# Kernel optimization log

Measured on AMD Instinct MI355X. Metric: run time of the kernel, lower is better.

Reference implementation:

```python
import jax, jax.numpy as jnp
import numpy as np

B, N, D = 4, 4096, 3
Q = jnp.array([0.05, 0.95, 0.25, 0.75], dtype=jnp.float32)  # q_begin + q_end


def _nn_diff(S1, S2):
    # For each point in S1 find nearest point in S2 (squared L2), return S1 - closest_S2.
    # d2: [N, N] built via the ||a||^2 + ||b||^2 - 2ab expansion (avoids [N,N,D]).
    d2 = (jnp.sum(S1 * S1, axis=-1, keepdims=True)
          + jnp.sum(S2 * S2, axis=-1)[None, :]
          - 2.0 * (S1 @ S2.T))
    idx = jnp.argmin(d2, axis=1)          # [N] nearest index in S2
    return S1 - S2[idx]                   # [N, D] vector residuals (mean=False path)


def _masked_std(v, mask):
    # torch.std over the masked subset (unbiased, correction=1), mask is float {0,1}.
    n = jnp.sum(mask)
    mean = jnp.sum(v * mask) / n
    var = jnp.sum(mask * (v - mean) ** 2) / (n - 1.0)
    return jnp.sqrt(var)


def _mask_std_pair(d):
    # mask_by_Z: quantiles computed under no_grad (stop_gradient), then std of each subset.
    v = d.reshape(-1)
    q = jnp.quantile(jax.lax.stop_gradient(v), Q.astype(v.dtype))
    mask_begin = ((v < q[0]) | (v > q[1])).astype(v.dtype)
    mask_end = ((v > q[2]) & (v < q[3])).astype(v.dtype)
    return _masked_std(v, mask_begin), _masked_std(v, mask_end)


def _sigma_distance(S1, S2):
    d12 = _nn_diff(S1, S2)  # S1 -> S2 residuals
    d21 = _nn_diff(S2, S1)  # S2 -> S1 residuals
    b1, e1 = _mask_std_pair(d12)
    b2, e2 = _mask_std_pair(d21)
    return jnp.maximum(b1, b2), jnp.maximum(e1, e2)


def setup_inputs() -> dict:
    key = jax.random.key(0)
    kx, ky = jax.random.split(key)
    x = jax.random.normal(kx, (B, N, D), dtype=jnp.float32)
    y = jax.random.normal(ky, (B, N, D), dtype=jnp.float32)
    return {"x": x, "y": y}


def reference(x, y):
    begin, end = jax.vmap(_sigma_distance)(x, y)  # [B], [B]
    return begin.mean(), end.mean()
```

## Files before the change

### kernel.cpp

```cpp
#include <hip/hip_runtime.h>
#include <math.h>

constexpr int B_  = 4;
constexpr int N_  = 4096;
constexpr int NV  = N_ * 3;
constexpr int QPT = 8;
constexpr int TPB_TAIL = 1024;

__device__ inline unsigned f2k(float f) {
    unsigned b = __float_as_uint(f);
    return b ^ ((unsigned)((int)b >> 31) | 0x80000000u);
}
__device__ inline float k2f(unsigned k) {
    unsigned b = (k & 0x80000000u) ? (k ^ 0x80000000u) : ~k;
    return __uint_as_float(b);
}

template <int NCCH>
__global__ __launch_bounds__(256, 2) void nn_partial_kernel(const float* __restrict__ x,
                                                            const float* __restrict__ y,
                                                            float2* __restrict__ part) {
    constexpr int CCH = N_ / NCCH;
    __shared__ float4 s2[CCH];
    const int pair = blockIdx.z;
    const int b    = pair >> 1;
    const int dir  = pair & 1;
    const float* S1 = (dir == 0 ? x : y) + b * NV;
    const float* S2 = (dir == 0 ? y : x) + b * NV;
    const int cbase = blockIdx.x * CCH;

    for (int j = threadIdx.x; j < CCH; j += 256) {
        float bx = S2[(cbase + j) * 3 + 0];
        float by = S2[(cbase + j) * 3 + 1];
        float bz = S2[(cbase + j) * 3 + 2];
        s2[j] = make_float4(-2.f * bx, -2.f * by, -2.f * bz,
                            bx * bx + by * by + bz * bz);
    }
    __syncthreads();

    const int q0 = blockIdx.y * 2048 + threadIdx.x * QPT;
    float ax[QPT], ay[QPT], az[QPT];
    {
        const float4* p4 = (const float4*)(S1 + q0 * 3);
        float4 v[6];
        #pragma unroll
        for (int i = 0; i < 6; ++i) v[i] = p4[i];
        const float* f = (const float*)v;
        #pragma unroll
        for (int k = 0; k < QPT; ++k) {
            ax[k] = f[k * 3 + 0]; ay[k] = f[k * 3 + 1]; az[k] = f[k * 3 + 2];
        }
    }

    float bd[QPT]; int idx[QPT];
    #pragma unroll
    for (int k = 0; k < QPT; ++k) { bd[k] = INFINITY; idx[k] = 0; }

    for (int j = 0; j < CCH; ++j) {
        float4 c = s2[j];
        asm volatile("" : "+v"(c.x), "+v"(c.y), "+v"(c.z), "+v"(c.w));
        const int jg = cbase + j;
        #pragma unroll
        for (int k = 0; k < QPT; ++k) {
            float d2 = fmaf(ax[k], c.x, fmaf(ay[k], c.y, fmaf(az[k], c.z, c.w)));
            if (d2 < bd[k]) idx[k] = jg;
            bd[k] = fminf(d2, bd[k]);
        }
    }

    float2 o[QPT];
    #pragma unroll
    for (int k = 0; k < QPT; ++k) o[k] = make_float2(bd[k], (float)idx[k]);
    float4* op = (float4*)(part + (size_t)(pair * NCCH + blockIdx.x) * N_ + q0);
    #pragma unroll
    for (int i = 0; i < QPT / 2; ++i) op[i] = ((const float4*)o)[i];
}

template <int NCCH>
__global__ __launch_bounds__(256) void merge_keys_kernel(const float* __restrict__ x,
                                                         const float* __restrict__ y,
                                                         const float2* __restrict__ part,
                                                         unsigned* __restrict__ keys) {
    const int pair = blockIdx.y;
    const int b    = pair >> 1;
    const int dir  = pair & 1;
    const float* S1 = (dir == 0 ? x : y) + b * NV;
    const float* S2 = (dir == 0 ? y : x) + b * NV;
    const int q = blockIdx.x * 256 + threadIdx.x;

    float best = INFINITY;
    int bidx = 0;
    #pragma unroll
    for (int c = 0; c < NCCH; ++c) {
        float2 p = part[(size_t)(pair * NCCH + c) * N_ + q];
        if (p.x < best) { best = p.x; bidx = (int)p.y; }
    }
    unsigned* kp = keys + (size_t)pair * NV;
    kp[0 * N_ + q] = f2k(S1[q * 3 + 0] - S2[bidx * 3 + 0]);
    kp[1 * N_ + q] = f2k(S1[q * 3 + 1] - S2[bidx * 3 + 1]);
    kp[2 * N_ + q] = f2k(S1[q * 3 + 2] - S2[bidx * 3 + 2]);
}

__global__ __launch_bounds__(TPB_TAIL) void tail_kernel(const unsigned* __restrict__ gkeys,
                                                        float* __restrict__ stats) {
    __shared__ unsigned keys[NV];
    __shared__ int hist8[8][256];
    __shared__ unsigned s_prefix[4];
    __shared__ int s_want[4];
    __shared__ int s_cnt[4];
    __shared__ unsigned s_mn[4];
    __shared__ float s_qv[4];
    __shared__ float red[64];
    __shared__ float sh[8];

    const int pair = blockIdx.x;
    const int tid  = threadIdx.x;
    const int lane = tid & 63;
    const int wid  = tid >> 6;

    const uint4* g4 = (const uint4*)(gkeys + (size_t)pair * NV);
    uint4* l4w = (uint4*)keys;
    #pragma unroll
    for (int i = 0; i < 3; ++i)
        l4w[i * TPB_TAIL + tid] = g4[i * TPB_TAIL + tid];
    if (tid < 4) {
        const float Qs[4] = {0.05f, 0.95f, 0.25f, 0.75f};
        s_prefix[tid] = 0u;
        s_want[tid]   = (int)floorf(Qs[tid] * (float)(NV - 1));
    }
    __syncthreads();

    const uint4* k4 = (const uint4*)keys;
    #pragma unroll 1
    for (int pass = 0; pass < 4; ++pass) {
        const int shift = 24 - 8 * pass;
        ((int*)hist8)[tid]             = 0;
        ((int*)hist8)[tid + TPB_TAIL]  = 0;
        __syncthreads();

        if (pass == 0) {
            int* h = hist8[wid & 7];
            for (int i = tid; i < NV / 4; i += TPB_TAIL) {
                uint4 kv = k4[i];
                atomicAdd(&h[kv.x >> 24], 1);
                atomicAdd(&h[kv.y >> 24], 1);
                atomicAdd(&h[kv.z >> 24], 1);
                atomicAdd(&h[kv.w >> 24], 1);
            }
        } else {
            const unsigned pmask = 0xFFFFFFFFu << (32 - 8 * pass);
            const unsigned pf0 = s_prefix[0], pf1 = s_prefix[1];
            const unsigned pf2 = s_prefix[2], pf3 = s_prefix[3];
            for (int i = tid; i < NV / 4; i += TPB_TAIL) {
                uint4 kv = k4[i];
                const unsigned ks[4] = {kv.x, kv.y, kv.z, kv.w};
                #pragma unroll
                for (int u = 0; u < 4; ++u) {
                    const unsigned k  = ks[u];
                    const unsigned kp = k & pmask;
                    const int bin = (int)((k >> shift) & 255u);
                    if (kp == pf0) atomicAdd(&hist8[0][bin], 1);
                    if (kp == pf1) atomicAdd(&hist8[1][bin], 1);
                    if (kp == pf2) atomicAdd(&hist8[2][bin], 1);
                    if (kp == pf3) atomicAdd(&hist8[3][bin], 1);
                }
            }
        }
        __syncthreads();

        if (wid < 4) {
            int c0 = 0, c1 = 0, c2 = 0, c3 = 0;
            if (pass == 0) {
                #pragma unroll
                for (int cp = 0; cp < 8; ++cp) {
                    c0 += hist8[cp][lane * 4 + 0]; c1 += hist8[cp][lane * 4 + 1];
                    c2 += hist8[cp][lane * 4 + 2]; c3 += hist8[cp][lane * 4 + 3];
                }
            } else {
                c0 = hist8[wid][lane * 4 + 0]; c1 = hist8[wid][lane * 4 + 1];
                c2 = hist8[wid][lane * 4 + 2]; c3 = hist8[wid][lane * 4 + 3];
            }
            const int want = s_want[wid];
            int s = c0 + c1 + c2 + c3;
            int pre = s;
            #pragma unroll
            for (int off = 1; off < 64; off <<= 1) {
                int u = __shfl_up(pre, off);
                if (lane >= off) pre += u;
            }
            const int excl = pre - s;
            const bool hit = (want >= excl) && (want < excl + s);
            unsigned long long m = __ballot(hit);
            const int hl = (int)(__ffsll(m) - 1);
            if (lane == hl) {
                int w = want - excl;
                int sel;
                if      (w < c0)           { sel = lane * 4 + 0; }
                else if (w < c0 + c1)      { sel = lane * 4 + 1; w -= c0; }
                else if (w < c0 + c1 + c2) { sel = lane * 4 + 2; w -= c0 + c1; }
                else                       { sel = lane * 4 + 3; w -= c0 + c1 + c2; }
                s_prefix[wid] |= ((unsigned)sel) << shift;
                s_want[wid] = w;
            }
        }
        __syncthreads();
    }

    if (tid < 4) { s_cnt[tid] = 0; s_mn[tid] = 0xFFFFFFFFu; }
    __syncthreads();
    const unsigned kq0 = s_prefix[0], kq1 = s_prefix[1];
    const unsigned kq2 = s_prefix[2], kq3 = s_prefix[3];
    int cnt0 = 0, cnt1 = 0, cnt2 = 0, cnt3 = 0;
    unsigned mn0 = 0xFFFFFFFFu, mn1 = 0xFFFFFFFFu, mn2 = 0xFFFFFFFFu, mn3 = 0xFFFFFFFFu;
    for (int i = tid; i < NV / 4; i += TPB_TAIL) {
        uint4 kv = k4[i];
        const unsigned ks[4] = {kv.x, kv.y, kv.z, kv.w};
        #pragma unroll
        for (int u = 0; u < 4; ++u) {
            const unsigned k = ks[u];
            if (k <= kq0) cnt0++; else if (k < mn0) mn0 = k;
            if (k <= kq1) cnt1++; else if (k < mn1) mn1 = k;
            if (k <= kq2) cnt2++; else if (k < mn2) mn2 = k;
            if (k <= kq3) cnt3++; else if (k < mn3) mn3 = k;
        }
    }
    #pragma unroll
    for (int off = 32; off > 0; off >>= 1) {
        cnt0 += __shfl_down(cnt0, off); cnt1 += __shfl_down(cnt1, off);
        cnt2 += __shfl_down(cnt2, off); cnt3 += __shfl_down(cnt3, off);
        unsigned u0 = __shfl_down(mn0, off); mn0 = u0 < mn0 ? u0 : mn0;
        unsigned u1 = __shfl_down(mn1, off); mn1 = u1 < mn1 ? u1 : mn1;
        unsigned u2 = __shfl_down(mn2, off); mn2 = u2 < mn2 ? u2 : mn2;
        unsigned u3 = __shfl_down(mn3, off); mn3 = u3 < mn3 ? u3 : mn3;
    }
    if (lane == 0) {
        atomicAdd(&s_cnt[0], cnt0); atomicMin(&s_mn[0], mn0);
        atomicAdd(&s_cnt[1], cnt1); atomicMin(&s_mn[1], mn1);
        atomicAdd(&s_cnt[2], cnt2); atomicMin(&s_mn[2], mn2);
        atomicAdd(&s_cnt[3], cnt3); atomicMin(&s_mn[3], mn3);
    }
    __syncthreads();
    if (tid < 4) {
        const float Qs[4] = {0.05f, 0.95f, 0.25f, 0.75f};
        const float pos = Qs[tid] * (float)(NV - 1);
        const int   k0  = (int)floorf(pos);
        const float fr  = pos - (float)k0;
        const float v0  = k2f(s_prefix[tid]);
        const float v1  = (s_cnt[tid] >= k0 + 2) ? v0 : k2f(s_mn[tid]);
        s_qv[tid] = v0 + fr * (v1 - v0);
    }
    __syncthreads();
    const float q0 = s_qv[0], q1 = s_qv[1], q2 = s_qv[2], q3 = s_qv[3];

    float cb = 0.f, sb = 0.f, ce = 0.f, se = 0.f;
    for (int i = tid; i < NV / 4; i += TPB_TAIL) {
        uint4 kv = k4[i];
        const unsigned ks[4] = {kv.x, kv.y, kv.z, kv.w};
        #pragma unroll
        for (int u = 0; u < 4; ++u) {
            const float val = k2f(ks[u]);
            if ((val < q0) || (val > q1)) { cb += 1.f; sb += val; }
            if ((val > q2) && (val < q3)) { ce += 1.f; se += val; }
        }
    }
    #pragma unroll
    for (int off = 32; off > 0; off >>= 1) {
        cb += __shfl_down(cb, off); sb += __shfl_down(sb, off);
        ce += __shfl_down(ce, off); se += __shfl_down(se, off);
    }
    if (lane == 0) {
        red[wid * 4 + 0] = cb; red[wid * 4 + 1] = sb;
        red[wid * 4 + 2] = ce; red[wid * 4 + 3] = se;
    }
    __syncthreads();
    if (tid == 0) {
        float tcb = 0.f, tsb = 0.f, tce = 0.f, tse = 0.f;
        for (int w = 0; w < 16; ++w) {
            tcb += red[w * 4 + 0]; tsb += red[w * 4 + 1];
            tce += red[w * 4 + 2]; tse += red[w * 4 + 3];
        }
        sh[0] = tsb / tcb;  sh[1] = tse / tce;
        sh[2] = tcb;        sh[3] = tce;
    }
    __syncthreads();
    const float mean_b = sh[0], mean_e = sh[1];
    const float nb = sh[2], ne = sh[3];

    float vb = 0.f, ve = 0.f;
    for (int i = tid; i < NV / 4; i += TPB_TAIL) {
        uint4 kv = k4[i];
        const unsigned ks[4] = {kv.x, kv.y, kv.z, kv.w};
        #pragma unroll
        for (int u = 0; u < 4; ++u) {
            const float val = k2f(ks[u]);
            if ((val < q0) || (val > q1)) { float d = val - mean_b; vb += d * d; }
            if ((val > q2) && (val < q3)) { float d = val - mean_e; ve += d * d; }
        }
    }
    #pragma unroll
    for (int off = 32; off > 0; off >>= 1) {
        vb += __shfl_down(vb, off);
        ve += __shfl_down(ve, off);
    }
    __syncthreads();
    if (lane == 0) { red[wid * 2 + 0] = vb; red[wid * 2 + 1] = ve; }
    __syncthreads();
    if (tid == 0) {
        float tvb = 0.f, tve = 0.f;
        for (int w = 0; w < 16; ++w) { tvb += red[w * 2 + 0]; tve += red[w * 2 + 1]; }
        stats[pair * 2 + 0] = sqrtf(tvb / (nb - 1.f));
        stats[pair * 2 + 1] = sqrtf(tve / (ne - 1.f));
    }
}

__global__ void final_kernel(const float* __restrict__ stats, float* __restrict__ out) {
    if (threadIdx.x == 0 && blockIdx.x == 0) {
        float sb = 0.f, se = 0.f;
        for (int b = 0; b < B_; ++b) {
            float b1 = stats[(b * 2 + 0) * 2 + 0];
            float b2 = stats[(b * 2 + 1) * 2 + 0];
            float e1 = stats[(b * 2 + 0) * 2 + 1];
            float e2 = stats[(b * 2 + 1) * 2 + 1];
            sb += fmaxf(b1, b2);
            se += fmaxf(e1, e2);
        }
        out[0] = sb / (float)B_;
        out[1] = se / (float)B_;
    }
}

template <int NCCH>
static void run_pipeline(const float* x, const float* y, float2* part,
                         unsigned* keys, float* stats, float* out,
                         hipStream_t stream) {
    nn_partial_kernel<NCCH><<<dim3(NCCH, 2, 8), 256, 0, stream>>>(x, y, part);
    merge_keys_kernel<NCCH><<<dim3(N_ / 256, 8), 256, 0, stream>>>(x, y, part, keys);
    tail_kernel<<<8, TPB_TAIL, 0, stream>>>(keys, stats);
    final_kernel<<<1, 64, 0, stream>>>(stats, out);
}

extern "C" void kernel_launch(void* const* d_in, const int* in_sizes, int n_in,
                              void* d_out, int out_size, void* d_ws, size_t ws_size,
                              hipStream_t stream) {
    const float* x = (const float*)d_in[0];
    const float* y = (const float*)d_in[1];
    float* out = (float*)d_out;

    unsigned* keys  = (unsigned*)d_ws;
    float*    stats = (float*)(keys + (size_t)8 * NV);
    float2*   part  = (float2*)(stats + 16);

    const size_t head   = ((size_t)8 * NV + 16) * sizeof(float);
    const size_t need32 = head + (size_t)8 * 32 * N_ * sizeof(float2);

    if (ws_size >= need32) {
        run_pipeline<32>(x, y, part, keys, stats, out, stream);
    } else {
        run_pipeline<8>(x, y, part, keys, stats, out, stream);
    }
}
```

Measured before the change: 70.22 us.

## Replace register-blocked shared-memory NN search with scalar per-query kernel and prescale pass

Adds a separate prescale kernel that turns each point into a (-2x,-2y,-2z,|p|^2) float4 once, instead of every block redoing it into shared memory. The nearest-neighbour kernel drops the 8-queries-per-thread register blocking and LDS staging: each thread now handles one query and streams candidates straight from global memory, all threads reading the same address. The candidate split is fixed at 16 chunks and the workspace-dependent template choice is removed. This raises the grid size for occupancy but gives up per-thread reuse of each candidate load across several queries, and adds one kernel launch.

```diff
diff --git a/kernel.cpp b/kernel.cpp
--- a/kernel.cpp
+++ b/kernel.cpp
@@ -4,7 +4,8 @@
 constexpr int B_  = 4;
 constexpr int N_  = 4096;
 constexpr int NV  = N_ * 3;
-constexpr int QPT = 8;
+constexpr int NCCH = 16;
+constexpr int CCH  = N_ / NCCH;
 constexpr int TPB_TAIL = 1024;
 
 __device__ inline unsigned f2k(float f) {
@@ -16,67 +17,49 @@
     return __uint_as_float(b);
 }
 
-template <int NCCH>
-__global__ __launch_bounds__(256, 2) void nn_partial_kernel(const float* __restrict__ x,
-                                                            const float* __restrict__ y,
-                                                            float2* __restrict__ part) {
-    constexpr int CCH = N_ / NCCH;
-    __shared__ float4 s2[CCH];
+__global__ __launch_bounds__(256) void prescale_kernel(const float* __restrict__ x,
+                                                       const float* __restrict__ y,
+                                                       float4* __restrict__ preX,
+                                                       float4* __restrict__ preY) {
+    const int t = blockIdx.x * 256 + threadIdx.x;
+    const float* src = blockIdx.y == 0 ? x : y;
+    float4* dst      = blockIdx.y == 0 ? preX : preY;
+    float bx = src[t * 3 + 0];
+    float by = src[t * 3 + 1];
+    float bz = src[t * 3 + 2];
+    dst[t] = make_float4(-2.f * bx, -2.f * by, -2.f * bz,
+                         bx * bx + by * by + bz * bz);
+}
+
+__global__ __launch_bounds__(256) void nn_scalar_kernel(const float* __restrict__ x,
+                                                        const float* __restrict__ y,
+                                                        const float4* __restrict__ preX,
+                                                        const float4* __restrict__ preY,
+                                                        float2* __restrict__ part) {
     const int pair = blockIdx.z;
     const int b    = pair >> 1;
     const int dir  = pair & 1;
-    const float* S1 = (dir == 0 ? x : y) + b * NV;
-    const float* S2 = (dir == 0 ? y : x) + b * NV;
+    const float*  S1 = (dir == 0 ? x : y) + b * NV;
+    const float4* P2 = (dir == 0 ? preY : preX) + b * N_;
     const int cbase = blockIdx.x * CCH;
 
-    for (int j = threadIdx.x; j < CCH; j += 256) {
-        float bx = S2[(cbase + j) * 3 + 0];
-        float by = S2[(cbase + j) * 3 + 1];
-        float bz = S2[(cbase + j) * 3 + 2];
-        s2[j] = make_float4(-2.f * bx, -2.f * by, -2.f * bz,
-                            bx * bx + by * by + bz * bz);
-    }
-    __syncthreads();
-
-    const int q0 = blockIdx.y * 2048 + threadIdx.x * QPT;
-    float ax[QPT], ay[QPT], az[QPT];
-    {
-        const float4* p4 = (const float4*)(S1 + q0 * 3);
-        float4 v[6];
-        #pragma unroll
-        for (int i = 0; i < 6; ++i) v[i] = p4[i];
-        const float* f = (const float*)v;
-        #pragma unroll
-        for (int k = 0; k < QPT; ++k) {
-            ax[k] = f[k * 3 + 0]; ay[k] = f[k * 3 + 1]; az[k] = f[k * 3 + 2];
-        }
-    }
-
-    float bd[QPT]; int idx[QPT];
-    #pragma unroll
-    for (int k = 0; k < QPT; ++k) { bd[k] = INFINITY; idx[k] = 0; }
-
+    const int q = blockIdx.y * 256 + threadIdx.x;
+    const float ax = S1[q * 3 + 0];
+    const float ay = S1[q * 3 + 1];
+    const float az = S1[q * 3 + 2];
+
+    float bd = INFINITY;
+    int idx = 0;
+    #pragma unroll 16
     for (int j = 0; j < CCH; ++j) {
-        float4 c = s2[j];
-        asm volatile("" : "+v"(c.x), "+v"(c.y), "+v"(c.z), "+v"(c.w));
-        const int jg = cbase + j;
-        #pragma unroll
-        for (int k = 0; k < QPT; ++k) {
-            float d2 = fmaf(ax[k], c.x, fmaf(ay[k], c.y, fmaf(az[k], c.z, c.w)));
-            if (d2 < bd[k]) idx[k] = jg;
-            bd[k] = fminf(d2, bd[k]);
-        }
-    }
-
-    float2 o[QPT];
-    #pragma unroll
-    for (int k = 0; k < QPT; ++k) o[k] = make_float2(bd[k], (float)idx[k]);
-    float4* op = (float4*)(part + (size_t)(pair * NCCH + blockIdx.x) * N_ + q0);
-    #pragma unroll
-    for (int i = 0; i < QPT / 2; ++i) op[i] = ((const float4*)o)[i];
-}
-
-template <int NCCH>
+        const float4 c = P2[cbase + j];
+        float d2 = fmaf(ax, c.x, fmaf(ay, c.y, fmaf(az, c.z, c.w)));
+        if (d2 < bd) idx = cbase + j;
+        bd = fminf(d2, bd);
+    }
+    part[(size_t)(pair * NCCH + blockIdx.x) * N_ + q] = make_float2(bd, (float)idx);
+}
+
 __global__ __launch_bounds__(256) void merge_keys_kernel(const float* __restrict__ x,
                                                          const float* __restrict__ y,
                                                          const float2* __restrict__ part,
@@ -329,16 +312,6 @@
     }
 }
 
-template <int NCCH>
-static void run_pipeline(const float* x, const float* y, float2* part,
-                         unsigned* keys, float* stats, float* out,
-                         hipStream_t stream) {
-    nn_partial_kernel<NCCH><<<dim3(NCCH, 2, 8), 256, 0, stream>>>(x, y, part);
-    merge_keys_kernel<NCCH><<<dim3(N_ / 256, 8), 256, 0, stream>>>(x, y, part, keys);
-    tail_kernel<<<8, TPB_TAIL, 0, stream>>>(keys, stats);
-    final_kernel<<<1, 64, 0, stream>>>(stats, out);
-}
-
 extern "C" void kernel_launch(void* const* d_in, const int* in_sizes, int n_in,
                               void* d_out, int out_size, void* d_ws, size_t ws_size,
                               hipStream_t stream) {
@@ -348,14 +321,13 @@
 
     unsigned* keys  = (unsigned*)d_ws;
     float*    stats = (float*)(keys + (size_t)8 * NV);
-    float2*   part  = (float2*)(stats + 16);
-
-    const size_t head   = ((size_t)8 * NV + 16) * sizeof(float);
-    const size_t need32 = head + (size_t)8 * 32 * N_ * sizeof(float2);
-
-    if (ws_size >= need32) {
-        run_pipeline<32>(x, y, part, keys, stats, out, stream);
-    } else {
-        run_pipeline<8>(x, y, part, keys, stats, out, stream);
-    }
-}
+    float4*   preX  = (float4*)(stats + 16);
+    float4*   preY  = preX + (size_t)B_ * N_;
+    float2*   part  = (float2*)(preY + (size_t)B_ * N_);
+
+    prescale_kernel<<<dim3(B_ * N_ / 256, 2), 256, 0, stream>>>(x, y, preX, preY);
+    nn_scalar_kernel<<<dim3(NCCH, N_ / 256, 8), 256, 0, stream>>>(x, y, preX, preY, part);
+    merge_keys_kernel<<<dim3(N_ / 256, 8), 256, 0, stream>>>(x, y, part, keys);
+    tail_kernel<<<8, TPB_TAIL, 0, stream>>>(keys, stats);
+    final_kernel<<<1, 64, 0, stream>>>(stats, out);
+}
```

New measurement: 65.65 us. 6.5% less time.
